# Kernel tuning notes

Measured on AMD Instinct MI355X. Metric: run time of the kernel, lower is better.

Reference implementation:

```python
import jax, jax.numpy as jnp
import numpy as np

VOCAB = 100000
HIDDEN = 128
BATCH = 2048


def setup_inputs() -> dict:
    key = jax.random.key(0)
    k1, k2, k3, k4, k5 = jax.random.split(key, 5)
    center_vec = jax.random.randint(k1, (BATCH,), 0, VOCAB)
    # nn.Linear(vocab, hidden): weight [hidden, vocab], bias [hidden]
    W_enc = jax.random.normal(k2, (HIDDEN, VOCAB), dtype=jnp.float32) * 0.02
    b_enc = jax.random.normal(k3, (HIDDEN,), dtype=jnp.float32) * 0.02
    # nn.Linear(hidden, vocab): weight [vocab, hidden], bias [vocab]
    W_dec = jax.random.normal(k4, (VOCAB, HIDDEN), dtype=jnp.float32) * 0.02
    b_dec = jax.random.normal(k5, (VOCAB,), dtype=jnp.float32) * 0.02
    return {"center_vec": center_vec, "W_enc": W_enc, "b_enc": b_enc,
            "W_dec": W_dec, "b_dec": b_dec}


def reference(center_vec, W_enc, b_enc, W_dec, b_dec):
    idx = center_vec.reshape(-1)  # [B]
    # one_hot @ W_enc^T + b_enc  ==  column-gather of W_enc  (same math, no one-hot)
    hidden = W_enc.T[idx] + b_enc                      # [B, H]
    logits = hidden @ W_dec.T + b_dec                  # [B, V]
    return jax.nn.log_softmax(logits, axis=1)
```

## Files before the change

### kernel.cpp

```cpp
#include <hip/hip_runtime.h>
#include <cstdint>
#include <cstddef>

#define V 100000
#define H 128
#define B 2048
#define NT 6250
#define CHUNK 50
#define NSTRIP 125
#define NRG 8

typedef __attribute__((ext_vector_type(8))) short short8;
typedef __attribute__((ext_vector_type(4))) float f32x4;

static __device__ __forceinline__ unsigned short f2bf(float f) {
  unsigned int u = __builtin_bit_cast(unsigned int, f);
  u += 0x7fffu + ((u >> 16) & 1u);
  return (unsigned short)(u >> 16);
}

__global__ void __launch_bounds__(256) prep_hidden(
    const int* __restrict__ idx, const float* __restrict__ W_enc,
    const float* __restrict__ b_enc, unsigned short* __restrict__ hid,
    float* __restrict__ accum) {
  int gid = blockIdx.x * 256 + threadIdx.x;
  if (gid < B) accum[gid] = 0.0f;
  if (gid >= B * H) return;
  int b = gid >> 7;
  int k = gid & (H - 1);
  float v = W_enc[(size_t)k * V + idx[b]] + b_enc[k];
  hid[gid] = f2bf(v);
}

__global__ void __launch_bounds__(256) cast_wdec_packed(
    const float* __restrict__ W, unsigned short* __restrict__ Wpk) {
  const int t = blockIdx.x;
  const int s = threadIdx.x >> 6;
  const int lane = threadIdx.x & 63;
  const int l15 = lane & 15;
  const int q = lane >> 4;
  const float* p = W + (size_t)(t * 16 + l15) * H + q * 8 + s * 32;
  float4 x = *reinterpret_cast<const float4*>(p);
  float4 y = *reinterpret_cast<const float4*>(p + 4);
  short8 o;
  o[0] = (short)f2bf(x.x); o[1] = (short)f2bf(x.y);
  o[2] = (short)f2bf(x.z); o[3] = (short)f2bf(x.w);
  o[4] = (short)f2bf(y.x); o[5] = (short)f2bf(y.y);
  o[6] = (short)f2bf(y.z); o[7] = (short)f2bf(y.w);
  *reinterpret_cast<short8*>(Wpk + (size_t)t * 2048 + s * 512 + lane * 8) = o;
}

template <bool PRE>
static __device__ __forceinline__ short8 loadW(const void* Wv, int t, int s,
                                               int lane, int l15, int q) {
  if constexpr (PRE) {
    return *reinterpret_cast<const short8*>(
        reinterpret_cast<const unsigned short*>(Wv) +
        (size_t)t * 2048 + s * 512 + lane * 8);
  } else {
    const float* p = reinterpret_cast<const float*>(Wv) +
                     (size_t)(t * 16 + l15) * H + q * 8 + s * 32;
    float4 x = *reinterpret_cast<const float4*>(p);
    float4 y = *reinterpret_cast<const float4*>(p + 4);
    short8 o;
    o[0] = (short)f2bf(x.x); o[1] = (short)f2bf(x.y);
    o[2] = (short)f2bf(x.z); o[3] = (short)f2bf(x.w);
    o[4] = (short)f2bf(y.x); o[5] = (short)f2bf(y.y);
    o[6] = (short)f2bf(y.z); o[7] = (short)f2bf(y.w);
    return o;
  }
}


template <bool PRE>
__global__ void __launch_bounds__(256) lse_pass(
    const void* __restrict__ Wv, const unsigned short* __restrict__ hid,
    const float* __restrict__ b_dec, float* __restrict__ accum) {
  const int lane = threadIdx.x & 63;
  const int wv = threadIdx.x >> 6;
  const int l15 = lane & 15;
  const int q = lane >> 4;
  const int rowbase = blockIdx.y * 256 + wv * 64;

  const unsigned short* ap = hid + (size_t)(rowbase + l15) * H + q * 8;
  short8 hf[4][4];
#pragma unroll
  for (int f = 0; f < 4; ++f)
#pragma unroll
    for (int s = 0; s < 4; ++s)
      hf[f][s] = *reinterpret_cast<const short8*>(ap + (size_t)f * 16 * H + s * 32);

  float ps[4] = {0.f, 0.f, 0.f, 0.f};

  const int t0 = blockIdx.x * CHUNK;
  const int t1 = t0 + CHUNK;

  short8 wb[4];
#pragma unroll
  for (int s = 0; s < 4; ++s) wb[s] = loadW<PRE>(Wv, t0, s, lane, l15, q);
  float4 bd4 = *reinterpret_cast<const float4*>(b_dec + t0 * 16 + q * 4);

#pragma unroll 2
  for (int t = t0; t < t1; ++t) {
    const int tn = (t + 1 < t1) ? t + 1 : t;
    short8 wn[4];
#pragma unroll
    for (int s = 0; s < 4; ++s) wn[s] = loadW<PRE>(Wv, tn, s, lane, l15, q);
    float4 bdn = *reinterpret_cast<const float4*>(b_dec + tn * 16 + q * 4);

#pragma unroll
    for (int f = 0; f < 4; ++f) {
      f32x4 acc = {0.f, 0.f, 0.f, 0.f};
#pragma unroll
      for (int s = 0; s < 4; ++s)
        acc = __builtin_amdgcn_mfma_f32_16x16x32_bf16(wb[s], hf[f][s], acc, 0, 0, 0);
      ps[f] += __expf(acc[0] + bd4.x) + __expf(acc[1] + bd4.y) +
               __expf(acc[2] + bd4.z) + __expf(acc[3] + bd4.w);
    }
#pragma unroll
    for (int s = 0; s < 4; ++s) wb[s] = wn[s];
    bd4 = bdn;
  }

#pragma unroll
  for (int f = 0; f < 4; ++f) {
    ps[f] += __shfl_xor(ps[f], 16, 64);
    ps[f] += __shfl_xor(ps[f], 32, 64);
    if (q == 0) atomicAdd(&accum[rowbase + f * 16 + l15], ps[f]);
  }
}

template <bool PRE>
__global__ void __launch_bounds__(256) out_pass(
    const void* __restrict__ Wv, const unsigned short* __restrict__ hid,
    const float* __restrict__ b_dec, const float* __restrict__ accum,
    float* __restrict__ out) {
  const int lane = threadIdx.x & 63;
  const int wv = threadIdx.x >> 6;
  const int l15 = lane & 15;
  const int q = lane >> 4;
  const int rowbase = blockIdx.y * 256 + wv * 64;

  const unsigned short* ap = hid + (size_t)(rowbase + l15) * H + q * 8;
  short8 hf[4][4];
#pragma unroll
  for (int f = 0; f < 4; ++f)
#pragma unroll
    for (int s = 0; s < 4; ++s)
      hf[f][s] = *reinterpret_cast<const short8*>(ap + (size_t)f * 16 * H + s * 32);

  const int t0 = blockIdx.x * CHUNK;

  float ls[4];
  size_t optr[4];
#pragma unroll
  for (int f = 0; f < 4; ++f) {
    ls[f] = __logf(accum[rowbase + f * 16 + l15]);
    optr[f] = (size_t)(rowbase + f * 16 + l15) * V + (size_t)t0 * 16 + q * 4;
  }

  short8 wa[4], wbv[4];
#pragma unroll
  for (int s = 0; s < 4; ++s) {
    wa[s] = loadW<PRE>(Wv, t0, s, lane, l15, q);
    wbv[s] = loadW<PRE>(Wv, t0 + 1, s, lane, l15, q);
  }
  float4 bda = *reinterpret_cast<const float4*>(b_dec + t0 * 16 + q * 4);
  float4 bdb = *reinterpret_cast<const float4*>(b_dec + (t0 + 1) * 16 + q * 4);

  const int NPAIR = CHUNK / 2;
  for (int tp = 0; tp < NPAIR; ++tp) {
    const int tpn = (tp + 1 < NPAIR) ? tp + 1 : tp;
    const int ta = t0 + 2 * tpn;
    short8 na[4], nb[4];
#pragma unroll
    for (int s = 0; s < 4; ++s) {
      na[s] = loadW<PRE>(Wv, ta, s, lane, l15, q);
      nb[s] = loadW<PRE>(Wv, ta + 1, s, lane, l15, q);
    }
    const float4 bna = *reinterpret_cast<const float4*>(b_dec + ta * 16 + q * 4);
    const float4 bnb = *reinterpret_cast<const float4*>(b_dec + (ta + 1) * 16 + q * 4);

#pragma unroll
    for (int f = 0; f < 4; ++f) {
      f32x4 acc0 = {0.f, 0.f, 0.f, 0.f};
      f32x4 acc1 = {0.f, 0.f, 0.f, 0.f};
#pragma unroll
      for (int s = 0; s < 4; ++s) {
        acc0 = __builtin_amdgcn_mfma_f32_16x16x32_bf16(wa[s], hf[f][s], acc0, 0, 0, 0);
        acc1 = __builtin_amdgcn_mfma_f32_16x16x32_bf16(wbv[s], hf[f][s], acc1, 0, 0, 0);
      }
      f32x4 o0, o1;
      o0[0] = acc0[0] + bda.x - ls[f];
      o0[1] = acc0[1] + bda.y - ls[f];
      o0[2] = acc0[2] + bda.z - ls[f];
      o0[3] = acc0[3] + bda.w - ls[f];
      o1[0] = acc1[0] + bdb.x - ls[f];
      o1[1] = acc1[1] + bdb.y - ls[f];
      o1[2] = acc1[2] + bdb.z - ls[f];
      o1[3] = acc1[3] + bdb.w - ls[f];
      float* p = out + optr[f];
      *reinterpret_cast<f32x4*>(p) = o0;
      *reinterpret_cast<f32x4*>(p + 16) = o1;
      optr[f] += 32;
    }
#pragma unroll
    for (int s = 0; s < 4; ++s) { wa[s] = na[s]; wbv[s] = nb[s]; }
    bda = bna;
    bdb = bnb;
  }
}

extern "C" void kernel_launch(void* const* d_in, const int* in_sizes, int n_in,
                              void* d_out, int out_size, void* d_ws, size_t ws_size,
                              hipStream_t stream) {
  const int* idx = (const int*)d_in[0];
  const float* W_enc = (const float*)d_in[1];
  const float* b_enc = (const float*)d_in[2];
  const float* W_dec = (const float*)d_in[3];
  const float* b_dec = (const float*)d_in[4];
  float* out = (float*)d_out;

  const size_t wb_bytes = (size_t)V * H * 2;
  const size_t hid_bytes = (size_t)B * H * 2;
  const bool pre = ws_size >= wb_bytes + hid_bytes + (size_t)B * 4;

  unsigned short* Wb;
  unsigned short* hid;
  float* accum;
  if (pre) {
    Wb = (unsigned short*)d_ws;
    hid = (unsigned short*)((char*)d_ws + wb_bytes);
    accum = (float*)((char*)d_ws + wb_bytes + hid_bytes);
  } else {
    Wb = nullptr;
    hid = (unsigned short*)d_ws;
    accum = (float*)((char*)d_ws + hid_bytes);
  }

  prep_hidden<<<dim3((B * H + 255) / 256), 256, 0, stream>>>(idx, W_enc, b_enc, hid, accum);

  if (pre) {
    cast_wdec_packed<<<dim3(NT), 256, 0, stream>>>(W_dec, Wb);
    lse_pass<true><<<dim3(NSTRIP, NRG), 256, 0, stream>>>((const void*)Wb, hid, b_dec, accum);
    out_pass<true><<<dim3(NSTRIP, NRG), 256, 0, stream>>>((const void*)Wb, hid, b_dec, accum, out);
  } else {
    lse_pass<false><<<dim3(NSTRIP, NRG), 256, 0, stream>>>((const void*)W_dec, hid, b_dec, accum);
    out_pass<false><<<dim3(NSTRIP, NRG), 256, 0, stream>>>((const void*)W_dec, hid, b_dec, accum, out);
  }
}
```

Before: 299.0 us.

## Enlarge vocab chunks, pair tiles in LSE pass, reorder output writes by row group

```diff
diff --git a/kernel.cpp b/kernel.cpp
--- a/kernel.cpp
+++ b/kernel.cpp
@@ -6,8 +6,8 @@
 #define H 128
 #define B 2048
 #define NT 6250
-#define CHUNK 50
-#define NSTRIP 125
+#define CHUNK 98
+#define NSTRIP 64
 #define NRG 8
 
 typedef __attribute__((ext_vector_type(8))) short short8;
@@ -93,33 +93,48 @@
   float ps[4] = {0.f, 0.f, 0.f, 0.f};
 
   const int t0 = blockIdx.x * CHUNK;
-  const int t1 = t0 + CHUNK;
-
-  short8 wb[4];
-#pragma unroll
-  for (int s = 0; s < 4; ++s) wb[s] = loadW<PRE>(Wv, t0, s, lane, l15, q);
-  float4 bd4 = *reinterpret_cast<const float4*>(b_dec + t0 * 16 + q * 4);
-
-#pragma unroll 2
-  for (int t = t0; t < t1; ++t) {
-    const int tn = (t + 1 < t1) ? t + 1 : t;
-    short8 wn[4];
-#pragma unroll
-    for (int s = 0; s < 4; ++s) wn[s] = loadW<PRE>(Wv, tn, s, lane, l15, q);
-    float4 bdn = *reinterpret_cast<const float4*>(b_dec + tn * 16 + q * 4);
+  const int t1 = (t0 + CHUNK < NT) ? t0 + CHUNK : NT;
+  const int np = (t1 - t0) >> 1;
+
+  short8 w0[4], w1[4];
+#pragma unroll
+  for (int s = 0; s < 4; ++s) {
+    w0[s] = loadW<PRE>(Wv, t0, s, lane, l15, q);
+    w1[s] = loadW<PRE>(Wv, t0 + 1, s, lane, l15, q);
+  }
+  float4 bd0 = *reinterpret_cast<const float4*>(b_dec + t0 * 16 + q * 4);
+  float4 bd1 = *reinterpret_cast<const float4*>(b_dec + (t0 + 1) * 16 + q * 4);
+
+  for (int p = 0; p < np; ++p) {
+    const int pn = (p + 1 < np) ? p + 1 : p;
+    const int ta = t0 + 2 * pn;
+    short8 n0[4], n1[4];
+#pragma unroll
+    for (int s = 0; s < 4; ++s) {
+      n0[s] = loadW<PRE>(Wv, ta, s, lane, l15, q);
+      n1[s] = loadW<PRE>(Wv, ta + 1, s, lane, l15, q);
+    }
+    const float4 bn0 = *reinterpret_cast<const float4*>(b_dec + ta * 16 + q * 4);
+    const float4 bn1 = *reinterpret_cast<const float4*>(b_dec + (ta + 1) * 16 + q * 4);
 
 #pragma unroll
     for (int f = 0; f < 4; ++f) {
-      f32x4 acc = {0.f, 0.f, 0.f, 0.f};
-#pragma unroll
-      for (int s = 0; s < 4; ++s)
-        acc = __builtin_amdgcn_mfma_f32_16x16x32_bf16(wb[s], hf[f][s], acc, 0, 0, 0);
-      ps[f] += __expf(acc[0] + bd4.x) + __expf(acc[1] + bd4.y) +
-               __expf(acc[2] + bd4.z) + __expf(acc[3] + bd4.w);
-    }
-#pragma unroll
-    for (int s = 0; s < 4; ++s) wb[s] = wn[s];
-    bd4 = bdn;
+      f32x4 a0 = {0.f, 0.f, 0.f, 0.f};
+      f32x4 a1 = {0.f, 0.f, 0.f, 0.f};
+#pragma unroll
+      for (int s = 0; s < 4; ++s) {
+        a0 = __builtin_amdgcn_mfma_f32_16x16x32_bf16(w0[s], hf[f][s], a0, 0, 0, 0);
+        a1 = __builtin_amdgcn_mfma_f32_16x16x32_bf16(w1[s], hf[f][s], a1, 0, 0, 0);
+      }
+      ps[f] += __expf(a0[0] + bd0.x) + __expf(a0[1] + bd0.y) +
+               __expf(a0[2] + bd0.z) + __expf(a0[3] + bd0.w) +
+               __expf(a1[0] + bd1.x) + __expf(a1[1] + bd1.y) +
+               __expf(a1[2] + bd1.z) + __expf(a1[3] + bd1.w);
+    }
+#pragma unroll
+    for (int s = 0; s < 4; ++s) { w0[s] = n0[s]; w1[s] = n1[s]; }
+    bd0 = bn0;
+    bd1 = bn1;
   }
 
 #pragma unroll
@@ -150,64 +165,60 @@
       hf[f][s] = *reinterpret_cast<const short8*>(ap + (size_t)f * 16 * H + s * 32);
 
   const int t0 = blockIdx.x * CHUNK;
+  const int t1 = (t0 + CHUNK < NT) ? t0 + CHUNK : NT;
 
   float ls[4];
-  size_t optr[4];
+  size_t rbase[4];
 #pragma unroll
   for (int f = 0; f < 4; ++f) {
     ls[f] = __logf(accum[rowbase + f * 16 + l15]);
-    optr[f] = (size_t)(rowbase + f * 16 + l15) * V + (size_t)t0 * 16 + q * 4;
-  }
-
-  short8 wa[4], wbv[4];
-#pragma unroll
-  for (int s = 0; s < 4; ++s) {
-    wa[s] = loadW<PRE>(Wv, t0, s, lane, l15, q);
-    wbv[s] = loadW<PRE>(Wv, t0 + 1, s, lane, l15, q);
-  }
-  float4 bda = *reinterpret_cast<const float4*>(b_dec + t0 * 16 + q * 4);
-  float4 bdb = *reinterpret_cast<const float4*>(b_dec + (t0 + 1) * 16 + q * 4);
-
-  const int NPAIR = CHUNK / 2;
-  for (int tp = 0; tp < NPAIR; ++tp) {
-    const int tpn = (tp + 1 < NPAIR) ? tp + 1 : tp;
-    const int ta = t0 + 2 * tpn;
-    short8 na[4], nb[4];
+    rbase[f] = (size_t)(rowbase + f * 16 + l15) * V;
+  }
+
+  auto pairbody = [&](int t, int f, float* op) {
+    short8 wa[4], wc[4];
 #pragma unroll
     for (int s = 0; s < 4; ++s) {
-      na[s] = loadW<PRE>(Wv, ta, s, lane, l15, q);
-      nb[s] = loadW<PRE>(Wv, ta + 1, s, lane, l15, q);
-    }
-    const float4 bna = *reinterpret_cast<const float4*>(b_dec + ta * 16 + q * 4);
-    const float4 bnb = *reinterpret_cast<const float4*>(b_dec + (ta + 1) * 16 + q * 4);
-
+      wa[s] = loadW<PRE>(Wv, t, s, lane, l15, q);
+      wc[s] = loadW<PRE>(Wv, t + 1, s, lane, l15, q);
+    }
+    const float4 bd0 = *reinterpret_cast<const float4*>(b_dec + t * 16 + q * 4);
+    const float4 bd1 = *reinterpret_cast<const float4*>(b_dec + (t + 1) * 16 + q * 4);
+    f32x4 a0 = {0.f, 0.f, 0.f, 0.f};
+    f32x4 a1 = {0.f, 0.f, 0.f, 0.f};
+#pragma unroll
+    for (int s = 0; s < 4; ++s) {
+      a0 = __builtin_amdgcn_mfma_f32_16x16x32_bf16(wa[s], hf[f][s], a0, 0, 0, 0);
+      a1 = __builtin_amdgcn_mfma_f32_16x16x32_bf16(wc[s], hf[f][s], a1, 0, 0, 0);
+    }
+    f32x4 o0, o1;
+    o0[0] = a0[0] + bd0.x - ls[f];
+    o0[1] = a0[1] + bd0.y - ls[f];
+    o0[2] = a0[2] + bd0.z - ls[f];
+    o0[3] = a0[3] + bd0.w - ls[f];
+    o1[0] = a1[0] + bd1.x - ls[f];
+    o1[1] = a1[1] + bd1.y - ls[f];
+    o1[2] = a1[2] + bd1.z - ls[f];
+    o1[3] = a1[3] + bd1.w - ls[f];
+    *reinterpret_cast<f32x4*>(op) = o0;
+    *reinterpret_cast<f32x4*>(op + 16) = o1;
+  };
+
+  for (int g = t0; g < t1; g += 8) {
+    const int ge = (g + 8 < t1) ? g + 8 : t1;
+    const int npr = (ge - g) >> 1;
 #pragma unroll
     for (int f = 0; f < 4; ++f) {
-      f32x4 acc0 = {0.f, 0.f, 0.f, 0.f};
-      f32x4 acc1 = {0.f, 0.f, 0.f, 0.f};
-#pragma unroll
-      for (int s = 0; s < 4; ++s) {
-        acc0 = __builtin_amdgcn_mfma_f32_16x16x32_bf16(wa[s], hf[f][s], acc0, 0, 0, 0);
-        acc1 = __builtin_amdgcn_mfma_f32_16x16x32_bf16(wbv[s], hf[f][s], acc1, 0, 0, 0);
+      float* op = out + rbase[f] + (size_t)g * 16 + q * 4;
+      if (npr == 4) {
+#pragma unroll 2
+        for (int pp = 0; pp < 4; ++pp)
+          pairbody(g + 2 * pp, f, op + pp * 32);
+      } else {
+        for (int pp = 0; pp < npr; ++pp)
+          pairbody(g + 2 * pp, f, op + pp * 32);
       }
-      f32x4 o0, o1;
-      o0[0] = acc0[0] + bda.x - ls[f];
-      o0[1] = acc0[1] + bda.y - ls[f];
-      o0[2] = acc0[2] + bda.z - ls[f];
-      o0[3] = acc0[3] + bda.w - ls[f];
-      o1[0] = acc1[0] + bdb.x - ls[f];
-      o1[1] = acc1[1] + bdb.y - ls[f];
-      o1[2] = acc1[2] + bdb.z - ls[f];
-      o1[3] = acc1[3] + bdb.w - ls[f];
-      float* p = out + optr[f];
-      *reinterpret_cast<f32x4*>(p) = o0;
-      *reinterpret_cast<f32x4*>(p + 16) = o1;
-      optr[f] += 32;
-    }
-#pragma unroll
-    for (int s = 0; s < 4; ++s) { wa[s] = na[s]; wbv[s] = nb[s]; }
-    bda = bna;
-    bdb = bnb;
+    }
   }
 }
 
```

After: 412.1 us. +37.8%, slower.

## Stage out_pass output tiles through LDS for row-contiguous global stores

Applied to the files above, without the earlier changes.

```diff
diff --git a/kernel.cpp b/kernel.cpp
--- a/kernel.cpp
+++ b/kernel.cpp
@@ -9,6 +9,8 @@
 #define CHUNK 50
 #define NSTRIP 125
 #define NRG 8
+#define ORG 16
+#define RS 68
 
 typedef __attribute__((ext_vector_type(8))) short short8;
 typedef __attribute__((ext_vector_type(4))) float f32x4;
@@ -131,15 +133,17 @@
 }
 
 template <bool PRE>
-__global__ void __launch_bounds__(256) out_pass(
+__global__ void __launch_bounds__(128) out_pass(
     const void* __restrict__ Wv, const unsigned short* __restrict__ hid,
     const float* __restrict__ b_dec, const float* __restrict__ accum,
     float* __restrict__ out) {
+  extern __shared__ float lds[];
   const int lane = threadIdx.x & 63;
   const int wv = threadIdx.x >> 6;
   const int l15 = lane & 15;
   const int q = lane >> 4;
-  const int rowbase = blockIdx.y * 256 + wv * 64;
+  const int rowbase = blockIdx.y * 128 + wv * 64;
+  float* sl = lds + wv * (64 * RS);
 
   const unsigned short* ap = hid + (size_t)(rowbase + l15) * H + q * 8;
   short8 hf[4][4];
@@ -152,12 +156,9 @@
   const int t0 = blockIdx.x * CHUNK;
 
   float ls[4];
-  size_t optr[4];
-#pragma unroll
-  for (int f = 0; f < 4; ++f) {
+#pragma unroll
+  for (int f = 0; f < 4; ++f)
     ls[f] = __logf(accum[rowbase + f * 16 + l15]);
-    optr[f] = (size_t)(rowbase + f * 16 + l15) * V + (size_t)t0 * 16 + q * 4;
-  }
 
   short8 wa[4], wbv[4];
 #pragma unroll
@@ -169,6 +170,7 @@
   float4 bdb = *reinterpret_cast<const float4*>(b_dec + (t0 + 1) * 16 + q * 4);
 
   const int NPAIR = CHUNK / 2;
+#pragma unroll 2
   for (int tp = 0; tp < NPAIR; ++tp) {
     const int tpn = (tp + 1 < NPAIR) ? tp + 1 : tp;
     const int ta = t0 + 2 * tpn;
@@ -181,6 +183,7 @@
     const float4 bna = *reinterpret_cast<const float4*>(b_dec + ta * 16 + q * 4);
     const float4 bnb = *reinterpret_cast<const float4*>(b_dec + (ta + 1) * 16 + q * 4);
 
+    const int pp = tp & 1;
 #pragma unroll
     for (int f = 0; f < 4; ++f) {
       f32x4 acc0 = {0.f, 0.f, 0.f, 0.f};
@@ -199,15 +202,39 @@
       o1[1] = acc1[1] + bdb.y - ls[f];
       o1[2] = acc1[2] + bdb.z - ls[f];
       o1[3] = acc1[3] + bdb.w - ls[f];
-      float* p = out + optr[f];
-      *reinterpret_cast<f32x4*>(p) = o0;
-      *reinterpret_cast<f32x4*>(p + 16) = o1;
-      optr[f] += 32;
-    }
+      float* sp = sl + (f * 16 + l15) * RS + pp * 32 + q * 4;
+      *reinterpret_cast<f32x4*>(sp) = o0;
+      *reinterpret_cast<f32x4*>(sp + 16) = o1;
+    }
+
+    if (pp == 1) {
+      const size_t gb = (size_t)(t0 + (tp >> 1) * 4) * 16;
+      const float* sr = sl + q * RS + l15 * 4;
+      float* ob = out + (size_t)(rowbase + q) * V + gb + l15 * 4;
+#pragma unroll
+      for (int rr = 0; rr < 64; rr += 4) {
+        f32x4 v = *reinterpret_cast<const f32x4*>(sr + rr * RS);
+        *reinterpret_cast<f32x4*>(ob + (size_t)rr * V) = v;
+      }
+    }
+
 #pragma unroll
     for (int s = 0; s < 4; ++s) { wa[s] = na[s]; wbv[s] = nb[s]; }
     bda = bna;
     bdb = bnb;
+  }
+
+  {
+    const size_t gb = (size_t)(t0 + 48) * 16;
+    if (l15 < 8) {
+      const float* sr = sl + q * RS + l15 * 4;
+      float* ob = out + (size_t)(rowbase + q) * V + gb + l15 * 4;
+#pragma unroll
+      for (int rr = 0; rr < 64; rr += 4) {
+        f32x4 v = *reinterpret_cast<const f32x4*>(sr + rr * RS);
+        *reinterpret_cast<f32x4*>(ob + (size_t)rr * V) = v;
+      }
+    }
   }
 }
 
@@ -224,6 +251,7 @@
   const size_t wb_bytes = (size_t)V * H * 2;
   const size_t hid_bytes = (size_t)B * H * 2;
   const bool pre = ws_size >= wb_bytes + hid_bytes + (size_t)B * 4;
+  const size_t out_lds = 2 * 64 * RS * sizeof(float);
 
   unsigned short* Wb;
   unsigned short* hid;
@@ -243,9 +271,9 @@
   if (pre) {
     cast_wdec_packed<<<dim3(NT), 256, 0, stream>>>(W_dec, Wb);
     lse_pass<true><<<dim3(NSTRIP, NRG), 256, 0, stream>>>((const void*)Wb, hid, b_dec, accum);
-    out_pass<true><<<dim3(NSTRIP, NRG), 256, 0, stream>>>((const void*)Wb, hid, b_dec, accum, out);
+    out_pass<true><<<dim3(NSTRIP, ORG), 128, out_lds, stream>>>((const void*)Wb, hid, b_dec, accum, out);
   } else {
     lse_pass<false><<<dim3(NSTRIP, NRG), 256, 0, stream>>>((const void*)W_dec, hid, b_dec, accum);
-    out_pass<false><<<dim3(NSTRIP, NRG), 256, 0, stream>>>((const void*)W_dec, hid, b_dec, accum, out);
-  }
-}
+    out_pass<false><<<dim3(NSTRIP, ORG), 128, out_lds, stream>>>((const void*)W_dec, hid, b_dec, accum, out);
+  }
+}
```

New measurement: 307.6 us. 2.9% more time.
